# Kernel tuning notes

Measured on AMD Instinct MI355X. Metric: run time of the kernel, lower is better.

The kernel has to match this reference:

```python
import jax, jax.numpy as jnp
import numpy as np

B, C, N, M, K = 1, 64, 65536, 65536, 16
H, O = 64, 128  # mlp hidden, out_channels


def setup_inputs() -> dict:
    key = jax.random.key(0)
    ks = jax.random.split(key, 8)
    return {
        "x": jax.random.normal(ks[0], (B, C, N), dtype=jnp.float32),
        "pos": jax.random.normal(ks[1], (B, 3, N), dtype=jnp.float32),
        "support_points": jax.random.normal(ks[2], (B, 3, M), dtype=jnp.float32),
        "W1": jax.random.normal(ks[3], (H, C + 3), dtype=jnp.float32) * 0.05,
        "b1": jax.random.normal(ks[4], (H,), dtype=jnp.float32) * 0.05,
        "W2": jax.random.normal(ks[5], (O, H), dtype=jnp.float32) * 0.05,
        "b2": jax.random.normal(ks[6], (O,), dtype=jnp.float32) * 0.05,
        "indices": jax.random.randint(ks[7], (B, M, K), 0, N, dtype=jnp.int64),
    }


def _gather_points(t, indices):
    # t: [B, C, N], indices: [B, M, K] -> [B, C, M, K]
    b, c, n = t.shape
    m, k = indices.shape[1], indices.shape[2]
    idx = indices.reshape(b, 1, m * k)  # broadcasts over channel dim
    return jnp.take_along_axis(t, idx, axis=2).reshape(b, c, m, k)


def reference(x, pos, support_points, W1, b1, W2, b2, indices):
    # gather neighbor features and positions: [B, C, M, K], [B, 3, M, K]
    feats = _gather_points(x, indices)
    pts = _gather_points(pos, indices) - support_points[:, :, :, None]
    h = jnp.concatenate([feats, pts], axis=1)  # [B, C+3, M, K]
    # shared per-point MLP (1x1 Conv2d == channel contraction)
    h = jnp.einsum("oc,bcmk->bomk", W1, h) + b1[None, :, None, None]
    h = jax.nn.relu(h)
    h = jnp.einsum("oc,bcmk->bomk", W2, h) + b2[None, :, None, None]
    # max-pool over neighborhood K -> [B, O, M]
    return jnp.max(h, axis=3)
```

## Files before the change

kernel.cpp:

```cpp
#include <hip/hip_runtime.h>

#define NPTS 65536
#define MPTS 65536
#define FSTR 72

typedef __attribute__((ext_vector_type(8))) short bf16x8;
typedef __attribute__((ext_vector_type(4))) float f32x4;

__device__ __forceinline__ float bflo(unsigned int u){ union{unsigned int i; float f;} v; v.i = u<<16; return v.f; }
__device__ __forceinline__ float bfhi(unsigned int u){ union{unsigned int i; float f;} v; v.i = u & 0xffff0000u; return v.f; }
__device__ __forceinline__ unsigned short f2bf(float f){
  union{float f; unsigned int i;} v; v.f=f;
  unsigned int r = v.i + 0x7fffu + ((v.i>>16)&1u);
  return (unsigned short)(r>>16);
}

#define MFMA32(a,b,c) __builtin_amdgcn_mfma_f32_16x16x32_bf16((a),(b),(c),0,0,0)

__global__ __launch_bounds__(256) void pack_all(
    const float* __restrict__ x, const float* __restrict__ pos,
    const float* __restrict__ W1, const float* __restrict__ W2,
    unsigned short* __restrict__ P2,
    unsigned short* __restrict__ W1F,
    unsigned short* __restrict__ W2F) {
  __shared__ unsigned int tile[64 * 37];
  const int t = threadIdx.x;
  const int n0 = blockIdx.x * 64;
  const int p = t & 63, cq = t >> 6;
  const int n = n0 + p;
  #pragma unroll
  for (int jj = 0; jj < 8; ++jj) {
    const int c = cq * 16 + 2 * jj;
    const unsigned int lo = f2bf(x[(size_t)c * NPTS + n]);
    const unsigned int hi = f2bf(x[(size_t)(c + 1) * NPTS + n]);
    tile[p * 37 + cq * 8 + jj] = lo | (hi << 16);
  }
  if (cq == 0) {
    const unsigned int a = f2bf(pos[n]);
    const unsigned int b = f2bf(pos[NPTS + n]);
    const unsigned int cc = f2bf(pos[2 * NPTS + n]);
    tile[p * 37 + 32] = a | (b << 16);
    tile[p * 37 + 33] = cc;
    tile[p * 37 + 34] = 0u;
    tile[p * 37 + 35] = 0u;
  }
  __syncthreads();
  unsigned int* Pd = (unsigned int*)(P2 + (size_t)n0 * FSTR);
  #pragma unroll
  for (int i = 0; i < 9; ++i) {
    const int u = t + i * 256;
    const int nl = u / 36, d = u - nl * 36;
    Pd[u] = tile[nl * 37 + d];
  }
  const int wid = blockIdx.x * 256 + t;
  if (wid < 768) {
    const int f = wid >> 6, lane = wid & 63;
    const int q = lane >> 4, lr = lane & 15;
    if (f < 8) {
      const int kt = f >> 2, nt = f & 3;
      #pragma unroll
      for (int j = 0; j < 8; ++j)
        W1F[wid*8 + j] = f2bf(W1[(nt*16 + lr)*67 + kt*32 + q*8 + j]);
    } else {
      const int nt = f - 8;
      #pragma unroll
      for (int j = 0; j < 8; ++j) {
        const int c = 64 + q*4 + j;
        W1F[wid*8 + j] = (j < 4 && c < 67) ? f2bf(W1[(nt*16 + lr)*67 + c]) : (unsigned short)0;
      }
    }
  } else if (wid < 768 + 1024) {
    const int gg = wid - 768;
    const int g = gg >> 6, lane = gg & 63;
    const int q = lane >> 4, lr = lane & 15;
    const int kt = g >> 3, ot = g & 7;
    #pragma unroll
    for (int j = 0; j < 8; ++j)
      W2F[gg*8 + j] = f2bf(W2[(ot*16 + lr)*64 + kt*32 + q*8 + j]);
  }
}

__global__ __launch_bounds__(256, 4) void pointnet_mfma(
    const unsigned short* __restrict__ P2,
    const float* __restrict__ sup,
    const unsigned short* __restrict__ W1F,
    const float* __restrict__ b1,
    const unsigned short* __restrict__ W2F,
    const float* __restrict__ b2,
    const int* __restrict__ indices,
    float* __restrict__ out) {
  __shared__ __align__(16) unsigned short featB[256 * FSTR];

  const int t = threadIdx.x;
  const int m0 = blockIdx.x * 16;
  const int lane = t & 63, w = t >> 6, quad = lane >> 4, lr = lane & 15;

  {
    const int idx = indices[m0*16 + t];
    const uint4* src = (const uint4*)(P2 + (size_t)idx * FSTR);
    uint4 u[9];
    #pragma unroll
    for (int i = 0; i < 9; ++i) u[i] = src[i];
    const int mm = m0 + (t >> 4);
    const float s0 = sup[mm], s1 = sup[MPTS + mm], s2 = sup[2*MPTS + mm];
    const float p0 = bflo(u[8].x), p1 = bfhi(u[8].x), p2 = bflo(u[8].y);
    u[8].x = (unsigned int)f2bf(p0 - s0) | ((unsigned int)f2bf(p1 - s1) << 16);
    u[8].y = (unsigned int)f2bf(p2 - s2);
    u[8].z = 0u; u[8].w = 0u;
    uint4* dst = (uint4*)(featB + t * FSTR);
    #pragma unroll
    for (int i = 0; i < 9; ++i) dst[i] = u[i];
  }

  const f32x4 fz = {0.f, 0.f, 0.f, 0.f};
  f32x4 acc1[4][4];
  #pragma unroll
  for (int nt = 0; nt < 4; ++nt)
    #pragma unroll
    for (int pt = 0; pt < 4; ++pt) acc1[nt][pt] = fz;

  #pragma unroll
  for (int kt = 0; kt < 2; ++kt) {
    bf16x8 wa[4];
    #pragma unroll
    for (int nt = 0; nt < 4; ++nt)
      wa[nt] = ((const bf16x8*)W1F)[(kt*4 + nt)*64 + lane];
    bf16x8 bfv[4];
    #pragma unroll
    for (int pt = 0; pt < 4; ++pt)
      bfv[pt] = *(const bf16x8*)&featB[(w*64 + pt*16 + lr)*FSTR + kt*32 + quad*8];
    #pragma unroll
    for (int nt = 0; nt < 4; ++nt)
      #pragma unroll
      for (int pt = 0; pt < 4; ++pt)
        acc1[nt][pt] = MFMA32(wa[nt], bfv[pt], acc1[nt][pt]);
  }
  {
    bf16x8 wa16[4];
    #pragma unroll
    for (int nt = 0; nt < 4; ++nt)
      wa16[nt] = ((const bf16x8*)W1F)[(8 + nt)*64 + lane];
    bf16x8 bt[4];
    #pragma unroll
    for (int pt = 0; pt < 4; ++pt)
      bt[pt] = *(const bf16x8*)&featB[(w*64 + pt*16 + lr)*FSTR + 64];
    #pragma unroll
    for (int nt = 0; nt < 4; ++nt)
      #pragma unroll
      for (int pt = 0; pt < 4; ++pt)
        acc1[nt][pt] = MFMA32(wa16[nt], bt[pt], acc1[nt][pt]);
  }

  #pragma unroll
  for (int nt = 0; nt < 4; ++nt) {
    const float4 bb = *(const float4*)(b1 + nt*16 + quad*4);
    #pragma unroll
    for (int pt = 0; pt < 4; ++pt) {
      const float v0 = fmaxf(acc1[nt][pt][0] + bb.x, 0.f);
      const float v1 = fmaxf(acc1[nt][pt][1] + bb.y, 0.f);
      const float v2 = fmaxf(acc1[nt][pt][2] + bb.z, 0.f);
      const float v3 = fmaxf(acc1[nt][pt][3] + bb.w, 0.f);
      uint2 d;
      d.x = (unsigned int)f2bf(v0) | ((unsigned int)f2bf(v1) << 16);
      d.y = (unsigned int)f2bf(v2) | ((unsigned int)f2bf(v3) << 16);
      *(uint2*)&featB[(w*64 + pt*16 + lr)*FSTR + nt*16 + quad*4] = d;
    }
  }

  bf16x8 ah[4][2];
  #pragma unroll
  for (int pt = 0; pt < 4; ++pt)
    #pragma unroll
    for (int kt = 0; kt < 2; ++kt)
      ah[pt][kt] = *(const bf16x8*)&featB[(w*64 + pt*16 + lr)*FSTR + kt*32 + quad*8];

  #pragma unroll
  for (int ot = 0; ot < 8; ++ot) {
    const bf16x8 wb0 = ((const bf16x8*)W2F)[(0*8 + ot)*64 + lane];
    const bf16x8 wb1 = ((const bf16x8*)W2F)[(1*8 + ot)*64 + lane];
    f32x4 a2[4];
    #pragma unroll
    for (int pt = 0; pt < 4; ++pt) {
      a2[pt] = MFMA32(ah[pt][0], wb0, fz);
      a2[pt] = MFMA32(ah[pt][1], wb1, a2[pt]);
    }
    float vm[4];
    #pragma unroll
    for (int pt = 0; pt < 4; ++pt) {
      float v = fmaxf(fmaxf(a2[pt][0], a2[pt][1]), fmaxf(a2[pt][2], a2[pt][3]));
      v = fmaxf(v, __shfl_xor(v, 16));
      v = fmaxf(v, __shfl_xor(v, 32));
      vm[pt] = v;
    }
    const float vq = (quad & 1) ? ((quad & 2) ? vm[3] : vm[1])
                                : ((quad & 2) ? vm[2] : vm[0]);
    const int o = ot*16 + lr;
    out[(size_t)o * MPTS + m0 + w*4 + quad] = vq + b2[o];
  }
}

__global__ __launch_bounds__(256) void pointnet_fallback(
    const float* __restrict__ x, const float* __restrict__ pos,
    const float* __restrict__ sup,
    const float* __restrict__ W1, const float* __restrict__ b1,
    const float* __restrict__ W2, const float* __restrict__ b2,
    const int* __restrict__ indices, float* __restrict__ out) {
  __shared__ float sfeat[16][68];
  __shared__ float shid[16][64];
  __shared__ float smax[4][128];
  __shared__ int sidx[16];
  const int t = threadIdx.x;
  const int m = blockIdx.x;
  if (t < 16) sidx[t] = indices[m*16 + t];
  const float sup0 = sup[m], sup1 = sup[MPTS + m], sup2 = sup[2*MPTS + m];
  __syncthreads();
  for (int u = t; u < 16*17; u += 256) {
    const int k = u / 17, c4 = (u - k*17) * 4;
    const int idx = sidx[k];
    float4 wv;
    if (c4 < 64) {
      wv.x = x[(size_t)(c4+0)*NPTS + idx]; wv.y = x[(size_t)(c4+1)*NPTS + idx];
      wv.z = x[(size_t)(c4+2)*NPTS + idx]; wv.w = x[(size_t)(c4+3)*NPTS + idx];
    } else {
      wv.x = pos[idx] - sup0; wv.y = pos[NPTS + idx] - sup1;
      wv.z = pos[2*NPTS + idx] - sup2; wv.w = 0.f;
    }
    *(float4*)&sfeat[k][c4] = wv;
  }
  const int h = t & 63, kg = t >> 6;
  float w1r[68];
  #pragma unroll
  for (int c = 0; c < 67; ++c) w1r[c] = W1[h*67 + c];
  w1r[67] = 0.f;
  const float bias1 = b1[h];
  __syncthreads();
  #pragma unroll
  for (int j = 0; j < 4; ++j) {
    const int k = kg*4 + j;
    float a = bias1;
    const float4* rr = (const float4*)sfeat[k];
    #pragma unroll
    for (int qq = 0; qq < 17; ++qq) {
      const float4 v = rr[qq];
      a += w1r[qq*4+0]*v.x + w1r[qq*4+1]*v.y + w1r[qq*4+2]*v.z + w1r[qq*4+3]*v.w;
    }
    shid[k][h] = fmaxf(a, 0.f);
  }
  const int ow = t & 63;
  float w2a[64], w2b[64];
  #pragma unroll
  for (int hh = 0; hh < 64; ++hh) { w2a[hh] = W2[ow*64 + hh]; w2b[hh] = W2[(ow+64)*64 + hh]; }
  __syncthreads();
  float mxa = -3.0e38f, mxb = -3.0e38f;
  #pragma unroll
  for (int j = 0; j < 4; ++j) {
    const int k = kg*4 + j;
    const float4* hr = (const float4*)shid[k];
    float pa = 0.f, pb = 0.f;
    #pragma unroll
    for (int qq = 0; qq < 16; ++qq) {
      const float4 v = hr[qq];
      pa += w2a[qq*4+0]*v.x + w2a[qq*4+1]*v.y + w2a[qq*4+2]*v.z + w2a[qq*4+3]*v.w;
      pb += w2b[qq*4+0]*v.x + w2b[qq*4+1]*v.y + w2b[qq*4+2]*v.z + w2b[qq*4+3]*v.w;
    }
    mxa = fmaxf(mxa, pa); mxb = fmaxf(mxb, pb);
  }
  smax[kg][ow] = mxa; smax[kg][64 + ow] = mxb;
  __syncthreads();
  if (t < 128) {
    out[(size_t)t * MPTS + m] =
        fmaxf(fmaxf(smax[0][t], smax[1][t]), fmaxf(smax[2][t], smax[3][t])) + b2[t];
  }
}

extern "C" void kernel_launch(void* const* d_in, const int* in_sizes, int n_in,
                              void* d_out, int out_size, void* d_ws, size_t ws_size,
                              hipStream_t stream) {
  const float* x   = (const float*)d_in[0];
  const float* pos = (const float*)d_in[1];
  const float* sup = (const float*)d_in[2];
  const float* W1  = (const float*)d_in[3];
  const float* b1  = (const float*)d_in[4];
  const float* W2  = (const float*)d_in[5];
  const float* b2  = (const float*)d_in[6];
  const int* indices = (const int*)d_in[7];
  float* out = (float*)d_out;

  const size_t P2_BYTES  = (size_t)NPTS * FSTR * 2;
  const size_t W1F_BYTES = 12 * 64 * 8 * 2;
  const size_t W2F_BYTES = 16 * 64 * 8 * 2;
  if (ws_size >= P2_BYTES + W1F_BYTES + W2F_BYTES) {
    unsigned short* P2  = (unsigned short*)d_ws;
    unsigned short* W1F = (unsigned short*)((char*)d_ws + P2_BYTES);
    unsigned short* W2F = (unsigned short*)((char*)d_ws + P2_BYTES + W1F_BYTES);
    pack_all<<<NPTS/64, 256, 0, stream>>>(x, pos, W1, W2, P2, W1F, W2F);
    pointnet_mfma<<<MPTS/16, 256, 0, stream>>>(P2, sup, W1F, b1, W2F, b2, indices, out);
  } else {
    pointnet_fallback<<<MPTS, 256, 0, stream>>>(x, pos, sup, W1, b1, W2, b2, indices, out);
  }
}
```

Before: 147.4 us.

## Precompute first MLP layer per source point and subtract support-point term after gather

Uses linearity of the first layer: W1·[x_n; pos_n - s_m] + b1 = (W1·[x_n; pos_n] + b1) - W1_pos·s_m. Layer 1 is therefore computed once per source point in a new pack kernel, instead of once per gathered neighbor. The main kernel gathers 64-wide pre-activations, subtracts the support-point term and applies ReLU before layer 2. This removes the 16x-redundant layer-1 MFMA work and shrinks gathered rows from 72 to 64 bf16. In exchange it adds an extra launch and per-thread scalar FMA work, and rounds the pre-activation to bf16 before the subtraction, which changes numerics slightly.

```diff
diff --git a/kernel.cpp b/kernel.cpp
--- a/kernel.cpp
+++ b/kernel.cpp
@@ -2,7 +2,6 @@
 
 #define NPTS 65536
 #define MPTS 65536
-#define FSTR 72
 
 typedef __attribute__((ext_vector_type(8))) short bf16x8;
 typedef __attribute__((ext_vector_type(4))) float f32x4;
@@ -14,45 +13,16 @@
   unsigned int r = v.i + 0x7fffu + ((v.i>>16)&1u);
   return (unsigned short)(r>>16);
 }
+__device__ __forceinline__ unsigned int pk2(float a, float b){
+  return (unsigned int)f2bf(a) | ((unsigned int)f2bf(b) << 16);
+}
 
 #define MFMA32(a,b,c) __builtin_amdgcn_mfma_f32_16x16x32_bf16((a),(b),(c),0,0,0)
 
-__global__ __launch_bounds__(256) void pack_all(
-    const float* __restrict__ x, const float* __restrict__ pos,
+__global__ __launch_bounds__(256) void pack_w(
     const float* __restrict__ W1, const float* __restrict__ W2,
-    unsigned short* __restrict__ P2,
-    unsigned short* __restrict__ W1F,
-    unsigned short* __restrict__ W2F) {
-  __shared__ unsigned int tile[64 * 37];
-  const int t = threadIdx.x;
-  const int n0 = blockIdx.x * 64;
-  const int p = t & 63, cq = t >> 6;
-  const int n = n0 + p;
-  #pragma unroll
-  for (int jj = 0; jj < 8; ++jj) {
-    const int c = cq * 16 + 2 * jj;
-    const unsigned int lo = f2bf(x[(size_t)c * NPTS + n]);
-    const unsigned int hi = f2bf(x[(size_t)(c + 1) * NPTS + n]);
-    tile[p * 37 + cq * 8 + jj] = lo | (hi << 16);
-  }
-  if (cq == 0) {
-    const unsigned int a = f2bf(pos[n]);
-    const unsigned int b = f2bf(pos[NPTS + n]);
-    const unsigned int cc = f2bf(pos[2 * NPTS + n]);
-    tile[p * 37 + 32] = a | (b << 16);
-    tile[p * 37 + 33] = cc;
-    tile[p * 37 + 34] = 0u;
-    tile[p * 37 + 35] = 0u;
-  }
-  __syncthreads();
-  unsigned int* Pd = (unsigned int*)(P2 + (size_t)n0 * FSTR);
-  #pragma unroll
-  for (int i = 0; i < 9; ++i) {
-    const int u = t + i * 256;
-    const int nl = u / 36, d = u - nl * 36;
-    Pd[u] = tile[nl * 37 + d];
-  }
-  const int wid = blockIdx.x * 256 + t;
+    unsigned short* __restrict__ W1F, unsigned short* __restrict__ W2F) {
+  const int wid = blockIdx.x * 256 + threadIdx.x;
   if (wid < 768) {
     const int f = wid >> 6, lane = wid & 63;
     const int q = lane >> 4, lr = lane & 15;
@@ -80,16 +50,91 @@
   }
 }
 
-__global__ __launch_bounds__(256, 4) void pointnet_mfma(
-    const unsigned short* __restrict__ P2,
-    const float* __restrict__ sup,
+__global__ __launch_bounds__(256) void pack_u(
+    const float* __restrict__ x,
+    const float* __restrict__ pos,
     const unsigned short* __restrict__ W1F,
     const float* __restrict__ b1,
+    unsigned short* __restrict__ U) {
+  const int t = threadIdx.x;
+  const int lane = t & 63, w = t >> 6, quad = lane >> 4, lr = lane & 15;
+  const int nb = blockIdx.x * 256 + w * 64;
+
+  bf16x8 wa[2][4], wt[4];
+  #pragma unroll
+  for (int kt = 0; kt < 2; ++kt)
+    #pragma unroll
+    for (int nt = 0; nt < 4; ++nt)
+      wa[kt][nt] = ((const bf16x8*)W1F)[(kt*4 + nt)*64 + lane];
+  #pragma unroll
+  for (int nt = 0; nt < 4; ++nt)
+    wt[nt] = ((const bf16x8*)W1F)[(8 + nt)*64 + lane];
+
+  const f32x4 fz = {0.f, 0.f, 0.f, 0.f};
+  f32x4 acc[4][4];
+  #pragma unroll
+  for (int nt = 0; nt < 4; ++nt)
+    #pragma unroll
+    for (int pt = 0; pt < 4; ++pt) acc[nt][pt] = fz;
+
+  #pragma unroll
+  for (int kt = 0; kt < 2; ++kt) {
+    bf16x8 bfr[4];
+    #pragma unroll
+    for (int pt = 0; pt < 4; ++pt) {
+      const float* xc = x + (size_t)(kt*32 + quad*8) * NPTS + nb + pt*16 + lr;
+      union { unsigned int d[4]; bf16x8 v; } mk;
+      #pragma unroll
+      for (int i = 0; i < 4; ++i)
+        mk.d[i] = pk2(xc[(size_t)(2*i) * NPTS], xc[(size_t)(2*i + 1) * NPTS]);
+      bfr[pt] = mk.v;
+    }
+    #pragma unroll
+    for (int nt = 0; nt < 4; ++nt)
+      #pragma unroll
+      for (int pt = 0; pt < 4; ++pt)
+        acc[nt][pt] = MFMA32(wa[kt][nt], bfr[pt], acc[nt][pt]);
+  }
+  {
+    bf16x8 btr[4];
+    #pragma unroll
+    for (int pt = 0; pt < 4; ++pt) {
+      const int n = nb + pt*16 + lr;
+      union { unsigned int d[4]; bf16x8 v; } mk;
+      mk.d[0] = pk2(pos[n], pos[NPTS + n]);
+      mk.d[1] = (unsigned int)f2bf(pos[2*NPTS + n]);
+      mk.d[2] = 0u; mk.d[3] = 0u;
+      btr[pt] = mk.v;
+    }
+    #pragma unroll
+    for (int nt = 0; nt < 4; ++nt)
+      #pragma unroll
+      for (int pt = 0; pt < 4; ++pt)
+        acc[nt][pt] = MFMA32(wt[nt], btr[pt], acc[nt][pt]);
+  }
+  #pragma unroll
+  for (int nt = 0; nt < 4; ++nt) {
+    const float4 bb = *(const float4*)(b1 + nt*16 + quad*4);
+    #pragma unroll
+    for (int pt = 0; pt < 4; ++pt) {
+      const int n = nb + pt*16 + lr;
+      uint2 d;
+      d.x = pk2(acc[nt][pt][0] + bb.x, acc[nt][pt][1] + bb.y);
+      d.y = pk2(acc[nt][pt][2] + bb.z, acc[nt][pt][3] + bb.w);
+      *(uint2*)(U + (size_t)n * 64 + nt*16 + quad*4) = d;
+    }
+  }
+}
+
+__global__ __launch_bounds__(256, 4) void pointnet_mfma2(
+    const unsigned short* __restrict__ U,
+    const float* __restrict__ sup,
+    const float* __restrict__ W1,
     const unsigned short* __restrict__ W2F,
     const float* __restrict__ b2,
     const int* __restrict__ indices,
     float* __restrict__ out) {
-  __shared__ __align__(16) unsigned short featB[256 * FSTR];
+  __shared__ __align__(16) unsigned short featB[256 * 72];
 
   const int t = threadIdx.x;
   const int m0 = blockIdx.x * 16;
@@ -97,83 +142,49 @@
 
   {
     const int idx = indices[m0*16 + t];
-    const uint4* src = (const uint4*)(P2 + (size_t)idx * FSTR);
-    uint4 u[9];
-    #pragma unroll
-    for (int i = 0; i < 9; ++i) u[i] = src[i];
-    const int mm = m0 + (t >> 4);
-    const float s0 = sup[mm], s1 = sup[MPTS + mm], s2 = sup[2*MPTS + mm];
-    const float p0 = bflo(u[8].x), p1 = bfhi(u[8].x), p2 = bflo(u[8].y);
-    u[8].x = (unsigned int)f2bf(p0 - s0) | ((unsigned int)f2bf(p1 - s1) << 16);
-    u[8].y = (unsigned int)f2bf(p2 - s2);
-    u[8].z = 0u; u[8].w = 0u;
-    uint4* dst = (uint4*)(featB + t * FSTR);
-    #pragma unroll
-    for (int i = 0; i < 9; ++i) dst[i] = u[i];
+    const uint4* src = (const uint4*)(U + (size_t)idx * 64);
+    uint4 u[8];
+    #pragma unroll
+    for (int i = 0; i < 8; ++i) u[i] = src[i];
+    uint4* dst = (uint4*)(featB + t * 72);
+    #pragma unroll
+    for (int i = 0; i < 8; ++i) dst[i] = u[i];
+  }
+
+  float w1p[16][3];
+  #pragma unroll
+  for (int kt = 0; kt < 2; ++kt)
+    #pragma unroll
+    for (int j = 0; j < 8; ++j) {
+      const float* r = W1 + (size_t)(kt*32 + quad*8 + j) * 67 + 64;
+      w1p[kt*8+j][0] = r[0]; w1p[kt*8+j][1] = r[1]; w1p[kt*8+j][2] = r[2];
+    }
+
+  bf16x8 ah[4][2];
+  #pragma unroll
+  for (int pt = 0; pt < 4; ++pt) {
+    const int m = m0 + w*4 + pt;
+    const float s0 = sup[m], s1 = sup[MPTS + m], s2 = sup[2*MPTS + m];
+    #pragma unroll
+    for (int kt = 0; kt < 2; ++kt) {
+      const uint4 ur = *(const uint4*)&featB[(w*64 + pt*16 + lr)*72 + kt*32 + quad*8];
+      const unsigned int uu[4] = {ur.x, ur.y, ur.z, ur.w};
+      union { unsigned int d[4]; bf16x8 v; } mk;
+      #pragma unroll
+      for (int i = 0; i < 4; ++i) {
+        const float* wl = w1p[kt*8 + 2*i];
+        const float* wh = w1p[kt*8 + 2*i + 1];
+        const float vl = wl[0]*s0 + wl[1]*s1 + wl[2]*s2;
+        const float vh = wh[0]*s0 + wh[1]*s1 + wh[2]*s2;
+        const float hl = fmaxf(bflo(uu[i]) - vl, 0.f);
+        const float hh = fmaxf(bfhi(uu[i]) - vh, 0.f);
+        mk.d[i] = pk2(hl, hh);
+      }
+      ah[pt][kt] = mk.v;
+    }
   }
 
   const f32x4 fz = {0.f, 0.f, 0.f, 0.f};
-  f32x4 acc1[4][4];
-  #pragma unroll
-  for (int nt = 0; nt < 4; ++nt)
-    #pragma unroll
-    for (int pt = 0; pt < 4; ++pt) acc1[nt][pt] = fz;
-
-  #pragma unroll
-  for (int kt = 0; kt < 2; ++kt) {
-    bf16x8 wa[4];
-    #pragma unroll
-    for (int nt = 0; nt < 4; ++nt)
-      wa[nt] = ((const bf16x8*)W1F)[(kt*4 + nt)*64 + lane];
-    bf16x8 bfv[4];
-    #pragma unroll
-    for (int pt = 0; pt < 4; ++pt)
-      bfv[pt] = *(const bf16x8*)&featB[(w*64 + pt*16 + lr)*FSTR + kt*32 + quad*8];
-    #pragma unroll
-    for (int nt = 0; nt < 4; ++nt)
-      #pragma unroll
-      for (int pt = 0; pt < 4; ++pt)
-        acc1[nt][pt] = MFMA32(wa[nt], bfv[pt], acc1[nt][pt]);
-  }
-  {
-    bf16x8 wa16[4];
-    #pragma unroll
-    for (int nt = 0; nt < 4; ++nt)
-      wa16[nt] = ((const bf16x8*)W1F)[(8 + nt)*64 + lane];
-    bf16x8 bt[4];
-    #pragma unroll
-    for (int pt = 0; pt < 4; ++pt)
-      bt[pt] = *(const bf16x8*)&featB[(w*64 + pt*16 + lr)*FSTR + 64];
-    #pragma unroll
-    for (int nt = 0; nt < 4; ++nt)
-      #pragma unroll
-      for (int pt = 0; pt < 4; ++pt)
-        acc1[nt][pt] = MFMA32(wa16[nt], bt[pt], acc1[nt][pt]);
-  }
-
-  #pragma unroll
-  for (int nt = 0; nt < 4; ++nt) {
-    const float4 bb = *(const float4*)(b1 + nt*16 + quad*4);
-    #pragma unroll
-    for (int pt = 0; pt < 4; ++pt) {
-      const float v0 = fmaxf(acc1[nt][pt][0] + bb.x, 0.f);
-      const float v1 = fmaxf(acc1[nt][pt][1] + bb.y, 0.f);
-      const float v2 = fmaxf(acc1[nt][pt][2] + bb.z, 0.f);
-      const float v3 = fmaxf(acc1[nt][pt][3] + bb.w, 0.f);
-      uint2 d;
-      d.x = (unsigned int)f2bf(v0) | ((unsigned int)f2bf(v1) << 16);
-      d.y = (unsigned int)f2bf(v2) | ((unsigned int)f2bf(v3) << 16);
-      *(uint2*)&featB[(w*64 + pt*16 + lr)*FSTR + nt*16 + quad*4] = d;
-    }
-  }
-
-  bf16x8 ah[4][2];
-  #pragma unroll
-  for (int pt = 0; pt < 4; ++pt)
-    #pragma unroll
-    for (int kt = 0; kt < 2; ++kt)
-      ah[pt][kt] = *(const bf16x8*)&featB[(w*64 + pt*16 + lr)*FSTR + kt*32 + quad*8];
-
   #pragma unroll
   for (int ot = 0; ot < 8; ++ot) {
     const bf16x8 wb0 = ((const bf16x8*)W2F)[(0*8 + ot)*64 + lane];
@@ -286,15 +297,16 @@
   const int* indices = (const int*)d_in[7];
   float* out = (float*)d_out;
 
-  const size_t P2_BYTES  = (size_t)NPTS * FSTR * 2;
+  const size_t U_BYTES   = (size_t)NPTS * 64 * 2;
   const size_t W1F_BYTES = 12 * 64 * 8 * 2;
   const size_t W2F_BYTES = 16 * 64 * 8 * 2;
-  if (ws_size >= P2_BYTES + W1F_BYTES + W2F_BYTES) {
-    unsigned short* P2  = (unsigned short*)d_ws;
-    unsigned short* W1F = (unsigned short*)((char*)d_ws + P2_BYTES);
-    unsigned short* W2F = (unsigned short*)((char*)d_ws + P2_BYTES + W1F_BYTES);
-    pack_all<<<NPTS/64, 256, 0, stream>>>(x, pos, W1, W2, P2, W1F, W2F);
-    pointnet_mfma<<<MPTS/16, 256, 0, stream>>>(P2, sup, W1F, b1, W2F, b2, indices, out);
+  if (ws_size >= U_BYTES + W1F_BYTES + W2F_BYTES) {
+    unsigned short* U   = (unsigned short*)d_ws;
+    unsigned short* W1F = (unsigned short*)((char*)d_ws + U_BYTES);
+    unsigned short* W2F = (unsigned short*)((char*)d_ws + U_BYTES + W1F_BYTES);
+    pack_w<<<7, 256, 0, stream>>>(W1, W2, W1F, W2F);
+    pack_u<<<NPTS/256, 256, 0, stream>>>(x, pos, W1F, b1, U);
+    pointnet_mfma2<<<MPTS/16, 256, 0, stream>>>(U, sup, W1, W2F, b2, indices, out);
   } else {
     pointnet_fallback<<<MPTS, 256, 0, stream>>>(x, pos, sup, W1, b1, W2, b2, indices, out);
   }
```

Result: faster. 142.9 us (-3.1%).
